# Kernel optimization log

Hardware: AMD Instinct MI355X
Metric: run time of the kernel (lower is better)

## Reference

```python
import jax, jax.numpy as jnp
import numpy as np

EPS = 1e-12  # matches torch F.normalize eps

def _l2norm(v, axis):
    return v / jnp.clip(jnp.linalg.norm(v, axis=axis, keepdims=True), EPS)

def setup_inputs() -> dict:
    key = jax.random.key(0)
    ks = jax.random.split(key, 5)
    B, D, H, W, K, OUT = 8, 512, 40, 40, 64, 4096
    x = jax.random.normal(ks[0], (B, D, H, W), dtype=jnp.float32)
    conv_w = jax.random.normal(ks[1], (K, D), dtype=jnp.float32) * (1.0 / np.sqrt(D))
    centers = jax.random.normal(ks[2], (D, K), dtype=jnp.float32)
    whiten_w = jax.random.normal(ks[3], (OUT, D * K), dtype=jnp.float32) * (1.0 / np.sqrt(D * K))
    whiten_b = jax.random.normal(ks[4], (OUT,), dtype=jnp.float32) * 0.01
    return {"x": x, "conv_w": conv_w, "centers": centers,
            "whiten_w": whiten_w, "whiten_b": whiten_b}

def reference(x, conv_w, centers, whiten_w, whiten_b):
    B, D = x.shape[0], x.shape[1]
    feat = x.reshape(B, D, -1)                       # [B, D, N]
    scores = jnp.einsum('kd,bdn->bkn', conv_w, feat)  # 1x1 Conv1d, no bias
    assign = jax.nn.softmax(scores, axis=1)           # softmax over clusters
    # vlad[b,d,k] = sum_n assign[b,k,n] * (feat[b,d,n] - centers[d,k])
    #            = (assign @ feat^T)[b,k,d]^T - (sum_n assign[b,k,n]) * centers[d,k]
    vlad = (jnp.einsum('bkn,bdn->bdk', assign, feat)
            - assign.sum(axis=-1)[:, None, :] * centers[None, :, :])  # [B, D, K]
    vlad = _l2norm(vlad, axis=1)                      # intra-normalization over D
    desc = vlad.reshape(B, -1)                        # [B, D*K]
    desc = _l2norm(desc, axis=1)
    desc = desc @ whiten_w.T + whiten_b               # whiten Linear -> [B, 4096]
    desc = _l2norm(desc, axis=1)
    return desc
```

## Files before the change

kernel.cpp:

```cpp
#include <hip/hip_runtime.h>

#define BB 8
#define DD 512
#define NPIX 1600
#define KK 64
#define OUTN 4096
#define DKN 32768
#define NSPLIT 25

__global__ __launch_bounds__(256) void k1_scores(
    const float* __restrict__ x, const float* __restrict__ convw,
    float* __restrict__ assignT, float* __restrict__ asum) {
  __shared__ float cws[64 * 68];
  __shared__ float xs[64 * 68];
  int t = threadIdx.x;
  int b = blockIdx.y;
  int n0 = blockIdx.x * 64;
  int tn = t & 15, tk = t >> 4;
  int r = t >> 2, c = (t & 3) * 16;
  float acc[4][4] = {};

  for (int d0 = 0; d0 < DD; d0 += 64) {
    const float* cw = convw + (long)r * DD + d0 + c;
    const float* xp = x + ((long)(b * DD + d0 + r)) * NPIX + n0 + c;
#pragma unroll
    for (int q = 0; q < 4; q++) {
      *(float4*)(&cws[r * 68 + c + q * 4]) = *(const float4*)(cw + q * 4);
      *(float4*)(&xs[r * 68 + c + q * 4]) = *(const float4*)(xp + q * 4);
    }
    __syncthreads();
#pragma unroll 4
    for (int dd = 0; dd < 64; ++dd) {
      float a0 = cws[(tk * 4 + 0) * 68 + dd];
      float a1 = cws[(tk * 4 + 1) * 68 + dd];
      float a2 = cws[(tk * 4 + 2) * 68 + dd];
      float a3 = cws[(tk * 4 + 3) * 68 + dd];
      float4 bv = *(const float4*)(&xs[dd * 68 + tn * 4]);
      acc[0][0] += a0 * bv.x; acc[0][1] += a0 * bv.y; acc[0][2] += a0 * bv.z; acc[0][3] += a0 * bv.w;
      acc[1][0] += a1 * bv.x; acc[1][1] += a1 * bv.y; acc[1][2] += a1 * bv.z; acc[1][3] += a1 * bv.w;
      acc[2][0] += a2 * bv.x; acc[2][1] += a2 * bv.y; acc[2][2] += a2 * bv.z; acc[2][3] += a2 * bv.w;
      acc[3][0] += a3 * bv.x; acc[3][1] += a3 * bv.y; acc[3][2] += a3 * bv.z; acc[3][3] += a3 * bv.w;
    }
    __syncthreads();
  }

#pragma unroll
  for (int i = 0; i < 4; i++)
#pragma unroll
    for (int j = 0; j < 4; j++)
      cws[(tn * 4 + j) * 68 + tk * 4 + i] = acc[i][j];
  __syncthreads();

  {
    int n = t >> 2;
    int kq = (t & 3) * 16;
    float v[16];
    float m = -1e30f;
#pragma unroll
    for (int q = 0; q < 4; q++) {
      float4 s4 = *(const float4*)(&cws[n * 68 + kq + q * 4]);
      v[q * 4 + 0] = s4.x; v[q * 4 + 1] = s4.y;
      v[q * 4 + 2] = s4.z; v[q * 4 + 3] = s4.w;
      m = fmaxf(m, fmaxf(fmaxf(s4.x, s4.y), fmaxf(s4.z, s4.w)));
    }
    m = fmaxf(m, __shfl_xor(m, 1, 64));
    m = fmaxf(m, __shfl_xor(m, 2, 64));
    float ssum = 0.f;
#pragma unroll
    for (int i = 0; i < 16; i++) {
      v[i] = expf(v[i] - m);
      ssum += v[i];
    }
    ssum += __shfl_xor(ssum, 1, 64);
    ssum += __shfl_xor(ssum, 2, 64);
    float inv = 1.0f / ssum;
    float* ap = assignT + ((long)b * NPIX + n0 + n) * KK + kq;
#pragma unroll
    for (int q = 0; q < 4; q++) {
      float4 o;
      o.x = v[q * 4 + 0] * inv; o.y = v[q * 4 + 1] * inv;
      o.z = v[q * 4 + 2] * inv; o.w = v[q * 4 + 3] * inv;
      *(float4*)(ap + q * 4) = o;
      *(float4*)(&cws[n * 68 + kq + q * 4]) = o;
    }
  }
  __syncthreads();
  {
    int k2i = t & 63, ng = t >> 6;
    float s = 0.f;
#pragma unroll
    for (int nn = ng * 16; nn < ng * 16 + 16; nn++) s += cws[nn * 68 + k2i];
    atomicAdd(&asum[b * KK + k2i], s);
  }
}

__global__ __launch_bounds__(256) void k2_vlad(
    const float* __restrict__ x, const float* __restrict__ assignT,
    float* __restrict__ vpT) {
  __shared__ float xs[64 * 68];
  __shared__ float as_[64 * 68];
  int t = threadIdx.x;
  int dt = blockIdx.x, ns = blockIdx.y, b = blockIdx.z;
  int d0 = dt * 64, n0 = ns * 64;
  int tk = t & 15, td = t >> 4;
  int r = t >> 2, c = (t & 3) * 16;
  float acc[4][4] = {};

  const float* xp = x + ((long)(b * DD + d0 + r)) * NPIX + n0 + c;
  const float* ap = assignT + ((long)b * NPIX + n0 + r) * KK + c;
#pragma unroll
  for (int q = 0; q < 4; q++) {
    *(float4*)(&xs[r * 68 + c + q * 4]) = *(const float4*)(xp + q * 4);
    *(float4*)(&as_[r * 68 + c + q * 4]) = *(const float4*)(ap + q * 4);
  }
  __syncthreads();
#pragma unroll 4
  for (int nn = 0; nn < 64; ++nn) {
    float a0 = xs[(td * 4 + 0) * 68 + nn];
    float a1 = xs[(td * 4 + 1) * 68 + nn];
    float a2 = xs[(td * 4 + 2) * 68 + nn];
    float a3 = xs[(td * 4 + 3) * 68 + nn];
    float4 bv = *(const float4*)(&as_[nn * 68 + tk * 4]);
    acc[0][0] += a0 * bv.x; acc[0][1] += a0 * bv.y; acc[0][2] += a0 * bv.z; acc[0][3] += a0 * bv.w;
    acc[1][0] += a1 * bv.x; acc[1][1] += a1 * bv.y; acc[1][2] += a1 * bv.z; acc[1][3] += a1 * bv.w;
    acc[2][0] += a2 * bv.x; acc[2][1] += a2 * bv.y; acc[2][2] += a2 * bv.z; acc[2][3] += a2 * bv.w;
    acc[3][0] += a3 * bv.x; acc[3][1] += a3 * bv.y; acc[3][2] += a3 * bv.z; acc[3][3] += a3 * bv.w;
  }
  float* vp = vpT + (((long)ns * BB + b) * KK) * DD;
#pragma unroll
  for (int j = 0; j < 4; j++) {
    int k = tk * 4 + j;
    float4 o = {acc[0][j], acc[1][j], acc[2][j], acc[3][j]};
    *(float4*)(vp + (long)k * DD + d0 + td * 4) = o;
  }
}

__global__ __launch_bounds__(256) void k3_norm(
    const float* __restrict__ vpT, const float* __restrict__ asum,
    const float* __restrict__ centers, float* __restrict__ desc,
    float* __restrict__ gsq) {
  __shared__ float sred[4];
  int k = blockIdx.x, b = blockIdx.y;
  int t = threadIdx.x;
  float a = asum[b * KK + k];
  float v[2];
#pragma unroll
  for (int h = 0; h < 2; h++) {
    int d = t + h * 256;
    float s = 0.f;
#pragma unroll 5
    for (int p = 0; p < NSPLIT; p++)
      s += vpT[(((long)p * BB + b) * KK + k) * DD + d];
    s -= a * centers[(long)d * KK + k];
    v[h] = s;
  }
  float ss = v[0] * v[0] + v[1] * v[1];
  for (int off = 32; off > 0; off >>= 1) ss += __shfl_down(ss, off, 64);
  if ((t & 63) == 0) sred[t >> 6] = ss;
  __syncthreads();
  float tot = sred[0] + sred[1] + sred[2] + sred[3];
  float sc = 1.0f / fmaxf(sqrtf(tot), 1e-12f);
#pragma unroll
  for (int h = 0; h < 2; h++) {
    int d = t + h * 256;
    desc[(long)b * DKN + (long)d * KK + k] = v[h] * sc;
  }
  if (t == 0) atomicAdd(&gsq[b], tot * sc * sc);
}

__global__ __launch_bounds__(256) void k4_whiten(
    const float* __restrict__ desc, const float* __restrict__ W,
    float* __restrict__ ydot) {
  int t = threadIdx.x;
  long o0 = (long)blockIdx.x * 8;
  int jbase = blockIdx.y * (DKN / 2);
  float acc[8][8];
#pragma unroll
  for (int oo = 0; oo < 8; oo++)
#pragma unroll
    for (int bb = 0; bb < 8; bb++) acc[oo][bb] = 0.f;

  const float* wbase = W + o0 * DKN;
  for (int jt = 0; jt < DKN / 2; jt += 1024) {
    int j = jbase + jt + t * 4;
    float4 d4[8];
#pragma unroll
    for (int bb = 0; bb < 8; bb++)
      d4[bb] = *(const float4*)(desc + (long)bb * DKN + j);
#pragma unroll
    for (int oo = 0; oo < 8; oo++) {
      float4 w4 = *(const float4*)(wbase + (long)oo * DKN + j);
#pragma unroll
      for (int bb = 0; bb < 8; bb++) {
        acc[oo][bb] += w4.x * d4[bb].x + w4.y * d4[bb].y +
                       w4.z * d4[bb].z + w4.w * d4[bb].w;
      }
    }
  }
  int lane = t & 63;
#pragma unroll
  for (int oo = 0; oo < 8; oo++)
#pragma unroll
    for (int bb = 0; bb < 8; bb++) {
      float v = acc[oo][bb];
      for (int off = 32; off > 0; off >>= 1) v += __shfl_down(v, off, 64);
      if (lane == 0) atomicAdd(&ydot[(long)bb * OUTN + o0 + oo], v);
    }
}

__global__ __launch_bounds__(256) void k5_final(
    const float* __restrict__ ydot, const float* __restrict__ gsq,
    const float* __restrict__ bias, float* __restrict__ out) {
  __shared__ float sred[4];
  int b = blockIdx.x, t = threadIdx.x;
  float g = fmaxf(sqrtf(gsq[b]), 1e-12f);
  float inv_g = 1.0f / g;
  float v[16];
  float ss = 0.f;
#pragma unroll
  for (int i = 0; i < 16; i++) {
    int o = t + i * 256;
    float val = ydot[(long)b * OUTN + o] * inv_g + bias[o];
    v[i] = val;
    ss += val * val;
  }
  for (int off = 32; off > 0; off >>= 1) ss += __shfl_down(ss, off, 64);
  if ((t & 63) == 0) sred[t >> 6] = ss;
  __syncthreads();
  float tot = sred[0] + sred[1] + sred[2] + sred[3];
  float sc = 1.0f / fmaxf(sqrtf(tot), 1e-12f);
#pragma unroll
  for (int i = 0; i < 16; i++) {
    int o = t + i * 256;
    out[(long)b * OUTN + o] = v[i] * sc;
  }
}

extern "C" void kernel_launch(void* const* d_in, const int* in_sizes, int n_in,
                              void* d_out, int out_size, void* d_ws,
                              size_t ws_size, hipStream_t stream) {
  const float* x = (const float*)d_in[0];
  const float* convw = (const float*)d_in[1];
  const float* centers = (const float*)d_in[2];
  const float* ww = (const float*)d_in[3];
  const float* wb = (const float*)d_in[4];
  float* out = (float*)d_out;

  float* base = (float*)d_ws;
  float* ydot = base;
  float* asum = base + 32768;
  float* gsq = base + 33280;
  float* assignT = base + 33288;
  float* desc = assignT;
  float* vpT = base + 33288 + 819200;

  hipMemsetAsync(base, 0, 33288 * sizeof(float), stream);

  hipLaunchKernelGGL(k1_scores, dim3(25, 8), dim3(256), 0, stream, x, convw,
                     assignT, asum);
  hipLaunchKernelGGL(k2_vlad, dim3(8, NSPLIT, 8), dim3(256), 0, stream, x,
                     assignT, vpT);
  hipLaunchKernelGGL(k3_norm, dim3(64, 8), dim3(256), 0, stream, vpT, asum,
                     centers, desc, gsq);
  hipLaunchKernelGGL(k4_whiten, dim3(512, 2), dim3(256), 0, stream, desc, ww,
                     ydot);
  hipLaunchKernelGGL(k5_final, dim3(8), dim3(256), 0, stream, ydot, gsq, wb,
                     out);
}
```

Measured before the change: 794.9 us.

## Transpose assignment layout, swizzle k2 tiles, halve N-splits, remove whiten atomics

k1 now writes the softmax assignments as [B,K,N] through a shared-memory transpose, so k2 can read both x and assign with float4 loads along N into an XOR-swizzled shared tile. Each k2 block now processes two N tiles, which halves the number of split partials that k3 has to sum. k4 reduces its partials across waves in shared memory and writes one result per split half with plain stores, and k5 adds the two halves. This replaces the global atomics and shrinks the memset. The cost is fewer k2 blocks, which lowers parallelism, and an extra transpose pass in k1.

```diff
diff --git a/kernel.cpp b/kernel.cpp
--- a/kernel.cpp
+++ b/kernel.cpp
@@ -6,13 +6,13 @@
 #define KK 64
 #define OUTN 4096
 #define DKN 32768
-#define NSPLIT 25
+#define NSPLIT 13
 
 __global__ __launch_bounds__(256) void k1_scores(
     const float* __restrict__ x, const float* __restrict__ convw,
-    float* __restrict__ assignT, float* __restrict__ asum) {
-  __shared__ float cws[64 * 68];
-  __shared__ float xs[64 * 68];
+    float* __restrict__ assign2, float* __restrict__ asum) {
+  __shared__ __align__(16) float cws[64 * 68];
+  __shared__ __align__(16) float xs[64 * 68];
   int t = threadIdx.x;
   int b = blockIdx.y;
   int n0 = blockIdx.x * 64;
@@ -74,13 +74,11 @@
     ssum += __shfl_xor(ssum, 1, 64);
     ssum += __shfl_xor(ssum, 2, 64);
     float inv = 1.0f / ssum;
-    float* ap = assignT + ((long)b * NPIX + n0 + n) * KK + kq;
 #pragma unroll
     for (int q = 0; q < 4; q++) {
       float4 o;
       o.x = v[q * 4 + 0] * inv; o.y = v[q * 4 + 1] * inv;
       o.z = v[q * 4 + 2] * inv; o.w = v[q * 4 + 3] * inv;
-      *(float4*)(ap + q * 4) = o;
       *(float4*)(&cws[n * 68 + kq + q * 4]) = o;
     }
   }
@@ -92,39 +90,66 @@
     for (int nn = ng * 16; nn < ng * 16 + 16; nn++) s += cws[nn * 68 + k2i];
     atomicAdd(&asum[b * KK + k2i], s);
   }
+  {
+    int k = t >> 2, g = t & 3;
+    float vv[16];
+#pragma unroll
+    for (int i = 0; i < 16; i++) vv[i] = cws[(g * 16 + i) * 68 + k];
+    float* ap = assign2 + ((long)b * KK + k) * NPIX + n0 + g * 16;
+#pragma unroll
+    for (int q = 0; q < 4; q++) {
+      float4 o4 = {vv[q * 4 + 0], vv[q * 4 + 1], vv[q * 4 + 2], vv[q * 4 + 3]};
+      *(float4*)(ap + q * 4) = o4;
+    }
+  }
 }
 
 __global__ __launch_bounds__(256) void k2_vlad(
-    const float* __restrict__ x, const float* __restrict__ assignT,
+    const float* __restrict__ x, const float* __restrict__ assign2,
     float* __restrict__ vpT) {
-  __shared__ float xs[64 * 68];
-  __shared__ float as_[64 * 68];
+  __shared__ __align__(16) float xs[64 * 68];
+  __shared__ __align__(16) float as_[64 * 64];
   int t = threadIdx.x;
   int dt = blockIdx.x, ns = blockIdx.y, b = blockIdx.z;
-  int d0 = dt * 64, n0 = ns * 64;
+  int d0 = dt * 64;
   int tk = t & 15, td = t >> 4;
   int r = t >> 2, c = (t & 3) * 16;
+  int sw = (tk & 7) << 2;
+  int swr = ((r >> 2) & 7) << 2;
   float acc[4][4] = {};
 
-  const float* xp = x + ((long)(b * DD + d0 + r)) * NPIX + n0 + c;
-  const float* ap = assignT + ((long)b * NPIX + n0 + r) * KK + c;
-#pragma unroll
-  for (int q = 0; q < 4; q++) {
-    *(float4*)(&xs[r * 68 + c + q * 4]) = *(const float4*)(xp + q * 4);
-    *(float4*)(&as_[r * 68 + c + q * 4]) = *(const float4*)(ap + q * 4);
-  }
-  __syncthreads();
-#pragma unroll 4
-  for (int nn = 0; nn < 64; ++nn) {
-    float a0 = xs[(td * 4 + 0) * 68 + nn];
-    float a1 = xs[(td * 4 + 1) * 68 + nn];
-    float a2 = xs[(td * 4 + 2) * 68 + nn];
-    float a3 = xs[(td * 4 + 3) * 68 + nn];
-    float4 bv = *(const float4*)(&as_[nn * 68 + tk * 4]);
-    acc[0][0] += a0 * bv.x; acc[0][1] += a0 * bv.y; acc[0][2] += a0 * bv.z; acc[0][3] += a0 * bv.w;
-    acc[1][0] += a1 * bv.x; acc[1][1] += a1 * bv.y; acc[1][2] += a1 * bv.z; acc[1][3] += a1 * bv.w;
-    acc[2][0] += a2 * bv.x; acc[2][1] += a2 * bv.y; acc[2][2] += a2 * bv.z; acc[2][3] += a2 * bv.w;
-    acc[3][0] += a3 * bv.x; acc[3][1] += a3 * bv.y; acc[3][2] += a3 * bv.z; acc[3][3] += a3 * bv.w;
+  for (int cc = 0; cc < 2; cc++) {
+    int nt = ns * 2 + cc;
+    if (nt >= 25) break;
+    int n0 = nt * 64;
+    const float* xp = x + ((long)(b * DD + d0 + r)) * NPIX + n0 + c;
+    const float* ap = assign2 + ((long)b * KK + r) * NPIX + n0 + c;
+#pragma unroll
+    for (int q = 0; q < 4; q++) {
+      *(float4*)(&xs[r * 68 + c + q * 4]) = *(const float4*)(xp + q * 4);
+      *(float4*)(&as_[r * 64 + ((c + q * 4) ^ swr)]) = *(const float4*)(ap + q * 4);
+    }
+    __syncthreads();
+#pragma unroll 2
+    for (int nn = 0; nn < 64; nn += 4) {
+      float4 xv0 = *(const float4*)(&xs[(td * 4 + 0) * 68 + nn]);
+      float4 xv1 = *(const float4*)(&xs[(td * 4 + 1) * 68 + nn]);
+      float4 xv2 = *(const float4*)(&xs[(td * 4 + 2) * 68 + nn]);
+      float4 xv3 = *(const float4*)(&xs[(td * 4 + 3) * 68 + nn]);
+      int nsw = nn ^ sw;
+      float4 av0 = *(const float4*)(&as_[(tk * 4 + 0) * 64 + nsw]);
+      float4 av1 = *(const float4*)(&as_[(tk * 4 + 1) * 64 + nsw]);
+      float4 av2 = *(const float4*)(&as_[(tk * 4 + 2) * 64 + nsw]);
+      float4 av3 = *(const float4*)(&as_[(tk * 4 + 3) * 64 + nsw]);
+#define DOT4(i, j, XV, AV) \
+  acc[i][j] += XV.x * AV.x + XV.y * AV.y + XV.z * AV.z + XV.w * AV.w
+      DOT4(0, 0, xv0, av0); DOT4(0, 1, xv0, av1); DOT4(0, 2, xv0, av2); DOT4(0, 3, xv0, av3);
+      DOT4(1, 0, xv1, av0); DOT4(1, 1, xv1, av1); DOT4(1, 2, xv1, av2); DOT4(1, 3, xv1, av3);
+      DOT4(2, 0, xv2, av0); DOT4(2, 1, xv2, av1); DOT4(2, 2, xv2, av2); DOT4(2, 3, xv2, av3);
+      DOT4(3, 0, xv3, av0); DOT4(3, 1, xv3, av1); DOT4(3, 2, xv3, av2); DOT4(3, 3, xv3, av3);
+#undef DOT4
+    }
+    __syncthreads();
   }
   float* vp = vpT + (((long)ns * BB + b) * KK) * DD;
 #pragma unroll
@@ -148,7 +173,7 @@
   for (int h = 0; h < 2; h++) {
     int d = t + h * 256;
     float s = 0.f;
-#pragma unroll 5
+#pragma unroll
     for (int p = 0; p < NSPLIT; p++)
       s += vpT[(((long)p * BB + b) * KK + k) * DD + d];
     s -= a * centers[(long)d * KK + k];
@@ -170,7 +195,8 @@
 
 __global__ __launch_bounds__(256) void k4_whiten(
     const float* __restrict__ desc, const float* __restrict__ W,
-    float* __restrict__ ydot) {
+    float* __restrict__ ydot2) {
+  __shared__ float red[256];
   int t = threadIdx.x;
   long o0 = (long)blockIdx.x * 8;
   int jbase = blockIdx.y * (DKN / 2);
@@ -197,19 +223,25 @@
       }
     }
   }
-  int lane = t & 63;
+  int lane = t & 63, w = t >> 6;
 #pragma unroll
   for (int oo = 0; oo < 8; oo++)
 #pragma unroll
     for (int bb = 0; bb < 8; bb++) {
       float v = acc[oo][bb];
       for (int off = 32; off > 0; off >>= 1) v += __shfl_down(v, off, 64);
-      if (lane == 0) atomicAdd(&ydot[(long)bb * OUTN + o0 + oo], v);
-    }
+      if (lane == 0) red[w * 64 + oo * 8 + bb] = v;
+    }
+  __syncthreads();
+  if (t < 64) {
+    int oo = t >> 3, bb = t & 7;
+    float s = red[t] + red[64 + t] + red[128 + t] + red[192 + t];
+    ydot2[((long)blockIdx.y * BB + bb) * OUTN + o0 + oo] = s;
+  }
 }
 
 __global__ __launch_bounds__(256) void k5_final(
-    const float* __restrict__ ydot, const float* __restrict__ gsq,
+    const float* __restrict__ ydot2, const float* __restrict__ gsq,
     const float* __restrict__ bias, float* __restrict__ out) {
   __shared__ float sred[4];
   int b = blockIdx.x, t = threadIdx.x;
@@ -220,7 +252,8 @@
 #pragma unroll
   for (int i = 0; i < 16; i++) {
     int o = t + i * 256;
-    float val = ydot[(long)b * OUTN + o] * inv_g + bias[o];
+    float dot = ydot2[(long)b * OUTN + o] + ydot2[((long)BB + b) * OUTN + o];
+    float val = dot * inv_g + bias[o];
     v[i] = val;
     ss += val * val;
   }
@@ -247,23 +280,23 @@
   float* out = (float*)d_out;
 
   float* base = (float*)d_ws;
-  float* ydot = base;
-  float* asum = base + 32768;
-  float* gsq = base + 33280;
-  float* assignT = base + 33288;
-  float* desc = assignT;
-  float* vpT = base + 33288 + 819200;
-
-  hipMemsetAsync(base, 0, 33288 * sizeof(float), stream);
+  float* asum = base;
+  float* gsq = base + 512;
+  float* ydot2 = base + 1024;
+  float* assign2 = base + 66560;
+  float* desc = assign2;
+  float* vpT = base + 66560 + 819200;
+
+  hipMemsetAsync(base, 0, 520 * sizeof(float), stream);
 
   hipLaunchKernelGGL(k1_scores, dim3(25, 8), dim3(256), 0, stream, x, convw,
-                     assignT, asum);
+                     assign2, asum);
   hipLaunchKernelGGL(k2_vlad, dim3(8, NSPLIT, 8), dim3(256), 0, stream, x,
-                     assignT, vpT);
+                     assign2, vpT);
   hipLaunchKernelGGL(k3_norm, dim3(64, 8), dim3(256), 0, stream, vpT, asum,
                      centers, desc, gsq);
   hipLaunchKernelGGL(k4_whiten, dim3(512, 2), dim3(256), 0, stream, desc, ww,
-                     ydot);
-  hipLaunchKernelGGL(k5_final, dim3(8), dim3(256), 0, stream, ydot, gsq, wb,
+                     ydot2);
+  hipLaunchKernelGGL(k5_final, dim3(8), dim3(256), 0, stream, ydot2, gsq, wb,
                      out);
 }
```

Measured after the change: 788.9 us. Within noise of the previous version (-0.7%).
